# Performance work log

Hardware: AMD Instinct MI355X
Metric: run time of the kernel (lower is better)

Reference implementation:

```python
import jax, jax.numpy as jnp
import numpy as np

N_NODES = 100000
N_EDGES = 1600000
D_FEAT = 128


def setup_inputs() -> dict:
    key = jax.random.key(0)
    k1, k2, k3, k4 = jax.random.split(key, 4)
    support = jax.random.normal(k1, (N_NODES, D_FEAT), dtype=jnp.float32)
    vals = jax.random.uniform(k2, (N_EDGES,), dtype=jnp.float32)
    rows = jax.random.randint(k3, (N_EDGES,), 0, N_NODES, dtype=jnp.int64)
    cols = jax.random.randint(k4, (N_EDGES,), 0, N_NODES, dtype=jnp.int64)
    return {"support": support, "vals": vals, "rows": rows, "cols": cols}


def reference(support, vals, rows, cols):
    # out = adj @ support, adj given in COO: adj[rows[e], cols[e]] = vals[e]
    # Gather neighbor features, scale by edge weight, scatter-add to row nodes.
    msgs = vals[:, None] * support[cols]          # [E, F]
    out = jax.ops.segment_sum(msgs, rows, num_segments=support.shape[0])  # [N, F]
    return out
```

## Files before the change

kernel.cpp:

```cpp
#include <hip/hip_runtime.h>
#include <hip/hip_bf16.h>
#include <hip/hip_fp16.h>


#define D_FEAT 128
#define F4 32
#define H4 32
#define H8 16
#define STRIDE 64
#define OVF_CAP 131072
#define EPT 8
#define BINT 1024
#define NBINS 1024
#define CAP 2048
#define GMAXIT 4
#define BROWS 100
#define GT 512
#define CSRCAP (CAP + 64)

typedef float    vfloat4 __attribute__((ext_vector_type(4)));
typedef _Float16 half4v  __attribute__((ext_vector_type(4)));
typedef _Float16 half8v  __attribute__((ext_vector_type(8)));


__global__ __launch_bounds__(BINT) void
phase1_bin_kernel(const float4* __restrict__ support4,
                  half8v* __restrict__ supporth,
                  const int* __restrict__ rows,
                  const int* __restrict__ cols,
                  const float* __restrict__ vals,
                  int2* __restrict__ dense,
                  int* __restrict__ gcur,
                  int4* __restrict__ ovf,
                  int* __restrict__ ovf_count,
                  int E, int BT, int NBLK, int n8) {
    int b = blockIdx.x;
    int tid = threadIdx.x;

    if (b >= NBLK) {
        int m = (b - NBLK) * BINT + tid;
        if (m < n8) {
            float4 a0 = support4[(size_t)m * 2];
            float4 a1 = support4[(size_t)m * 2 + 1];
            half8v h;
            h[0] = (_Float16)a0.x; h[1] = (_Float16)a0.y;
            h[2] = (_Float16)a0.z; h[3] = (_Float16)a0.w;
            h[4] = (_Float16)a1.x; h[5] = (_Float16)a1.y;
            h[6] = (_Float16)a1.z; h[7] = (_Float16)a1.w;
            supporth[m] = h;
        }
        return;
    }

    __shared__ int  hist[NBINS];
    __shared__ int  off[NBINS + 1];
    __shared__ int  sstart[NBINS];
    __shared__ int2 sorted[BINT * EPT];

    for (int i = tid; i < NBINS; i += BINT) hist[i] = 0;
    __syncthreads();

    int t = b * BINT + tid;
    int   r[EPT];
    int   c[EPT];
    float v[EPT];
    int   rk[EPT];

    #pragma unroll
    for (int i = 0; i < EPT; ++i) {
        int e = t + i * BT;
        r[i] = (e < E) ? rows[e] : -1;
    }
    #pragma unroll
    for (int i = 0; i < EPT; ++i) {
        int e = t + i * BT;
        if (e < E) { c[i] = cols[e]; v[i] = vals[e]; }
    }
    #pragma unroll
    for (int i = 0; i < EPT; ++i)
        rk[i] = (r[i] >= 0) ? atomicAdd(&hist[r[i] / BROWS], 1) : 0;
    __syncthreads();

    if (tid < 64) {
        int l[16];
        int s = 0;
        #pragma unroll
        for (int k = 0; k < 16; ++k) {
            l[k] = hist[tid * 16 + k];
            s += l[k];
        }
        int inc = s;
        #pragma unroll
        for (int dd = 1; dd < 64; dd <<= 1) {
            int tt = __shfl_up(inc, dd, 64);
            if (tid >= dd) inc += tt;
        }
        int run = inc - s;
        #pragma unroll
        for (int k = 0; k < 16; ++k) {
            off[tid * 16 + k] = run;
            run += l[k];
        }
        if (tid == 63) off[NBINS] = run;
    }
    __syncthreads();

    #pragma unroll
    for (int i = 0; i < EPT; ++i) {
        if (r[i] < 0) continue;
        int d = r[i] / BROWS;
        int2 q;
        q.x = ((r[i] - d * BROWS) << 17) | c[i];
        q.y = __float_as_int(v[i]);
        sorted[off[d] + rk[i]] = q;
    }
    __syncthreads();

    {
        int l = off[tid + 1] - off[tid];
        sstart[tid] = (l > 0) ? atomicAdd(&gcur[tid], l) : 0;
    }
    __syncthreads();

    {
        int grp  = tid >> 4;
        int lane = tid & 15;
        for (int d = grp; d < NBINS; d += 64) {
            int o  = off[d];
            int l  = off[d + 1] - o;
            int st = sstart[d];
            for (int k = lane; k < l; k += 16) {
                int pos = st + k;
                int2 q = sorted[o + k];
                if (pos < CAP) {
                    dense[(size_t)d * CAP + pos] = q;
                } else {
                    int ox = atomicAdd(ovf_count, 1);
                    if (ox < OVF_CAP) {
                        int4 e4;
                        e4.x = d * BROWS + ((q.x >> 17) & 255);
                        e4.y = q.x & 0x1FFFF;
                        e4.z = q.y;
                        e4.w = 0;
                        ovf[ox] = e4;
                    }
                }
            }
        }
    }
}


__global__ __launch_bounds__(GT) void
bucket_csr_gather_kernel(const half8v* __restrict__ supporth,
                         const int2* __restrict__ dense,
                         const int* __restrict__ gcur,
                         const int4* __restrict__ ovf,
                         const int* __restrict__ ovf_count,
                         float4* __restrict__ out4, int N) {
    __shared__ __align__(16) int cnt[128];
    __shared__ __align__(16) int oc[128];
    __shared__ int oc2[128];
    __shared__ int off[129];
    __shared__ int2 csr[CSRCAP + 8];

    const int d   = blockIdx.x;
    const int tid = threadIdx.x;
    const int2* dbase = dense + (size_t)d * CAP;
    const int base = d * BROWS;

    int total = gcur[d];
    if (total > CAP) total = CAP;
    int ocnt = *ovf_count;
    if (ocnt > OVF_CAP) ocnt = OVF_CAP;

    if (tid < 128) { cnt[tid] = 0; oc[tid] = 0; oc2[tid] = 0; }
    __syncthreads();

    int2 ent[GMAXIT];
    int  err[GMAXIT];
    int  ernk[GMAXIT];
    #pragma unroll
    for (int it = 0; it < GMAXIT; ++it) {
        int s = tid + it * GT;
        err[it] = -1;
        if (s < total) {
            int2 q = dbase[s];
            int r = (q.x >> 17) & 255;
            ent[it].x = q.x & 0x1FFFF;
            ent[it].y = q.y;
            err[it] = r;
            ernk[it] = atomicAdd(&cnt[r], 1);
        }
    }
    if (ocnt > 0) {
        for (int i = tid; i < ocnt; i += GT) {
            int rr = ovf[i].x - base;
            if (rr >= 0 && rr < BROWS) atomicAdd(&oc[rr], 1);
        }
    }
    __syncthreads();

    if (tid < 32) {
        int4 c4 = ((int4*)cnt)[tid];
        int4 o4 = ((int4*)oc)[tid];
        int t0 = c4.x + o4.x;
        int t1 = t0 + c4.y + o4.y;
        int t2 = t1 + c4.z + o4.z;
        int t3 = t2 + c4.w + o4.w;
        int inc = t3;
        #pragma unroll
        for (int dd = 1; dd < 32; dd <<= 1) {
            int t = __shfl_up(inc, dd, 32);
            if (tid >= dd) inc += t;
        }
        int excl = inc - t3;
        off[tid * 4 + 0] = excl;
        off[tid * 4 + 1] = excl + t0;
        off[tid * 4 + 2] = excl + t1;
        off[tid * 4 + 3] = excl + t2;
        if (tid == 31) off[128] = inc;
    }
    __syncthreads();

    #pragma unroll
    for (int it = 0; it < GMAXIT; ++it) {
        if (err[it] >= 0)
            csr[off[err[it]] + ernk[it]] = ent[it];
    }
    if (ocnt > 0) {
        for (int i = tid; i < ocnt; i += GT) {
            int4 q = ovf[i];
            int rr = q.x - base;
            if (rr >= 0 && rr < BROWS) {
                int idx = off[rr] + cnt[rr] + atomicAdd(&oc2[rr], 1);
                if (idx < CSRCAP) { int2 e; e.x = q.y; e.y = q.z; csr[idx] = e; }
            }
        }
    }
    __syncthreads();

    const int g = tid >> 4;
    const int i = tid & 15;
    for (int rq = 0; rq < 4; ++rq) {
        int r = rq * 32 + g;
        if (r >= BROWS) continue;
        int beg = off[r];
        int end = off[r + 1];
        vfloat4 a00 = {0.f,0.f,0.f,0.f}, a01 = {0.f,0.f,0.f,0.f};
        vfloat4 a10 = {0.f,0.f,0.f,0.f}, a11 = {0.f,0.f,0.f,0.f};
        for (int k0 = beg; k0 < end; k0 += 8) {
            int   cc[8];
            float vv[8];
            #pragma unroll
            for (int u = 0; u < 8; ++u) {
                int2 e = csr[k0 + u];
                bool ib = (k0 + u) < end;
                cc[u] = ib ? e.x : 0;
                vv[u] = ib ? __int_as_float(e.y) : 0.f;
            }
            half8v s[8];
            #pragma unroll
            for (int u = 0; u < 8; ++u)
                s[u] = supporth[(size_t)cc[u] * H8 + i];
            #pragma unroll
            for (int u = 0; u < 8; ++u) {
                float v = vv[u];
                if (u & 1) {
                    a10.x += v * (float)s[u][0];
                    a10.y += v * (float)s[u][1];
                    a10.z += v * (float)s[u][2];
                    a10.w += v * (float)s[u][3];
                    a11.x += v * (float)s[u][4];
                    a11.y += v * (float)s[u][5];
                    a11.z += v * (float)s[u][6];
                    a11.w += v * (float)s[u][7];
                } else {
                    a00.x += v * (float)s[u][0];
                    a00.y += v * (float)s[u][1];
                    a00.z += v * (float)s[u][2];
                    a00.w += v * (float)s[u][3];
                    a01.x += v * (float)s[u][4];
                    a01.y += v * (float)s[u][5];
                    a01.z += v * (float)s[u][6];
                    a01.w += v * (float)s[u][7];
                }
            }
        }
        int row = base + r;
        if (row < N) {
            vfloat4 r0, r1;
            r0.x = a00.x + a10.x; r0.y = a00.y + a10.y;
            r0.z = a00.z + a10.z; r0.w = a00.w + a10.w;
            r1.x = a01.x + a11.x; r1.y = a01.y + a11.y;
            r1.z = a01.z + a11.z; r1.w = a01.w + a11.w;
            float4* dst = &out4[(size_t)row * F4 + (i << 1)];
            __builtin_nontemporal_store(r0, (vfloat4*)dst);
            __builtin_nontemporal_store(r1, (vfloat4*)(dst + 1));
        }
    }
}


__global__ void ovf_scatter_kernel(const float* __restrict__ support,
                                   const int4* __restrict__ ovf,
                                   const int* __restrict__ ovf_count,
                                   float* __restrict__ out, int cap) {
    int gid = blockIdx.x * blockDim.x + threadIdx.x;
    int i = gid >> 5;
    int j = gid & 31;
    int istride = (gridDim.x * blockDim.x) >> 5;
    int cnt = *ovf_count;
    if (cnt > cap) cnt = cap;
    for (; i < cnt; i += istride) {
        int4 q = ovf[i];
        float v = __int_as_float(q.z);
        const float4* s4 = (const float4*)support + (size_t)q.y * F4 + j;
        float4 s = *s4;
        float* o = out + (size_t)q.x * D_FEAT + j * 4;
        unsafeAtomicAdd(o + 0, v * s.x);
        unsafeAtomicAdd(o + 1, v * s.y);
        unsafeAtomicAdd(o + 2, v * s.z);
        unsafeAtomicAdd(o + 3, v * s.w);
    }
}


__global__ void convert_kernel(const float4* __restrict__ in,
                               half8v* __restrict__ out, int n8) {
    int t = blockIdx.x * blockDim.x + threadIdx.x;
    if (t >= n8) return;
    float4 a = in[(size_t)t * 2];
    float4 b = in[(size_t)t * 2 + 1];
    half8v h;
    h[0] = (_Float16)a.x; h[1] = (_Float16)a.y;
    h[2] = (_Float16)a.z; h[3] = (_Float16)a.w;
    h[4] = (_Float16)b.x; h[5] = (_Float16)b.y;
    h[6] = (_Float16)b.z; h[7] = (_Float16)b.w;
    out[t] = h;
}

__global__ void gather_half_kernel(const half4v* __restrict__ supporth,
                                   const int* __restrict__ cursor,
                                   const int2* __restrict__ pairs,
                                   float4* __restrict__ out4, int n_nodes) {
    unsigned int t = blockIdx.x * blockDim.x + threadIdx.x;
    unsigned int row = t >> 5;
    unsigned int j = t & 31;
    if (row >= (unsigned int)n_nodes) return;
    int deg = cursor[row];
    if (deg > STRIDE) deg = STRIDE;
    const int2* pr = pairs + (size_t)row * STRIDE;
    int2 z = {0, 0};
    int2 p0 = ((int)j < deg) ? pr[j] : z;
    int2 p1 = ((int)(j + 32) < deg) ? pr[j + 32] : z;
    int   c0 = p0.x;  float v0 = __int_as_float(p0.y);
    int   c1 = p1.x;  float v1 = __int_as_float(p1.y);
    int degr = (deg + 7) & ~7;
    float4 acc[4];
    #pragma unroll
    for (int u = 0; u < 4; ++u) acc[u] = {0.f, 0.f, 0.f, 0.f};
    for (int k = 0; k < degr; k += 8) {
        int   cc[8];
        float vv[8];
        #pragma unroll
        for (int u = 0; u < 8; ++u) {
            int kk = k + u;
            cc[u] = __shfl(kk < 32 ? c0 : c1, kk & 31, 32);
            vv[u] = __shfl(kk < 32 ? v0 : v1, kk & 31, 32);
        }
        half4v s[8];
        #pragma unroll
        for (int u = 0; u < 8; ++u)
            s[u] = supporth[(size_t)cc[u] * H4 + j];
        #pragma unroll
        for (int u = 0; u < 8; ++u) {
            acc[u & 3].x += vv[u] * (float)s[u][0];
            acc[u & 3].y += vv[u] * (float)s[u][1];
            acc[u & 3].z += vv[u] * (float)s[u][2];
            acc[u & 3].w += vv[u] * (float)s[u][3];
        }
    }
    vfloat4 res;
    res.x = (acc[0].x + acc[1].x) + (acc[2].x + acc[3].x);
    res.y = (acc[0].y + acc[1].y) + (acc[2].y + acc[3].y);
    res.z = (acc[0].z + acc[1].z) + (acc[2].z + acc[3].z);
    res.w = (acc[0].w + acc[1].w) + (acc[2].w + acc[3].w);
    __builtin_nontemporal_store(res, (vfloat4*)&out4[(size_t)row * F4 + j]);
}

__global__ void bucket_ilp_kernel(const int* __restrict__ rows,
                                  const int* __restrict__ cols,
                                  const float* __restrict__ vals,
                                  int* __restrict__ cursor,
                                  int* __restrict__ ovf_count,
                                  int2* __restrict__ pairs,
                                  int4* __restrict__ ovf,
                                  int n_edges, int gstride) {
    int tid = blockIdx.x * blockDim.x + threadIdx.x;
    int   r[EPT];
    int   c[EPT];
    float v[EPT];
    int   slot[EPT];
    #pragma unroll
    for (int i = 0; i < EPT; ++i) {
        int e = tid + i * gstride;
        r[i] = (e < n_edges) ? rows[e] : -1;
    }
    #pragma unroll
    for (int i = 0; i < EPT; ++i) {
        int e = tid + i * gstride;
        if (e < n_edges) { c[i] = cols[e]; v[i] = vals[e]; }
    }
    #pragma unroll
    for (int i = 0; i < EPT; ++i)
        slot[i] = (r[i] >= 0) ? atomicAdd(&cursor[r[i]], 1) : 0;
    #pragma unroll
    for (int i = 0; i < EPT; ++i) {
        if (r[i] < 0) continue;
        int2 p;
        p.x = c[i];
        p.y = __float_as_int(v[i]);
        if (slot[i] < STRIDE) {
            pairs[(size_t)r[i] * STRIDE + slot[i]] = p;
        } else {
            int o = atomicAdd(ovf_count, 1);
            if (o < OVF_CAP) {
                int4 q; q.x = r[i]; q.y = p.x; q.z = p.y; q.w = 0;
                ovf[o] = q;
            }
        }
    }
}


__global__ void gc_scatter_kernel(const float* __restrict__ support,
                                  const float* __restrict__ vals,
                                  const int* __restrict__ rows,
                                  const int* __restrict__ cols,
                                  float* __restrict__ out, int n_edges) {
    unsigned int t = blockIdx.x * blockDim.x + threadIdx.x;
    unsigned int e = t >> 5;
    unsigned int j = t & 31;
    if (e >= (unsigned int)n_edges) return;
    int r = rows[e];
    int c = cols[e];
    float v = vals[e];
    const float4* s4 = reinterpret_cast<const float4*>(support) + (size_t)c * F4 + j;
    float4 s = *s4;
    float* o = out + (size_t)r * D_FEAT + j * 4;
    unsafeAtomicAdd(o + 0, v * s.x);
    unsafeAtomicAdd(o + 1, v * s.y);
    unsafeAtomicAdd(o + 2, v * s.z);
    unsafeAtomicAdd(o + 3, v * s.w);
}


extern "C" void kernel_launch(void* const* d_in, const int* in_sizes, int n_in,
                              void* d_out, int out_size, void* d_ws, size_t ws_size,
                              hipStream_t stream) {
    const float* support = (const float*)d_in[0];
    const float* vals    = (const float*)d_in[1];
    const int*   rows    = (const int*)d_in[2];
    const int*   cols    = (const int*)d_in[3];
    float* out = (float*)d_out;

    int E = in_sizes[1];
    int N = in_sizes[0] / D_FEAT;
    int n8 = N * D_FEAT / 8;
    int ND = (N + BROWS - 1) / BROWS;
    int NBLK = (E + BINT * EPT - 1) / (BINT * EPT);
    int BT = NBLK * BINT;

    char* ws = (char*)d_ws;
    size_t cur = 0;
    auto carve = [&](size_t bytes) -> void* {
        void* p = ws + cur;
        cur += (bytes + 255) & ~(size_t)255;
        return p;
    };

    {
        size_t save = cur;
        int2*   dense     = (int2*)carve((size_t)NBINS * CAP * 8);
        int*    gcur      = (int*)carve((size_t)(NBINS + 256) * 4);
        int4*   ovf       = (int4*)carve((size_t)OVF_CAP * 16);
        half8v* supporth  = (half8v*)carve((size_t)N * D_FEAT * 2);
        if (cur <= ws_size && ND <= NBINS) {
            int* ovf_count = gcur + NBINS;
            (void)hipMemsetAsync(gcur, 0, (size_t)(NBINS + 1) * 4, stream);
            int cblocks = (n8 + BINT - 1) / BINT;
            phase1_bin_kernel<<<NBLK + cblocks, BINT, 0, stream>>>(
                (const float4*)support, supporth, rows, cols, vals,
                dense, gcur, ovf, ovf_count, E, BT, NBLK, n8);
            bucket_csr_gather_kernel<<<ND, GT, 0, stream>>>(
                supporth, dense, gcur, ovf, ovf_count, (float4*)out, N);
            return;
        }
        cur = save;
    }

    {
        size_t save = cur;
        int*    cursor   = (int*)carve((size_t)(N + 1) * 4);
        int2*   pairs    = (int2*)carve((size_t)N * STRIDE * 8);
        int4*   ovf      = (int4*)carve((size_t)8192 * 16);
        half8v* supporth = (half8v*)carve((size_t)N * D_FEAT * 2);
        if (cur <= ws_size) {
            int* ovf_count = cursor + N;
            int bthreads = (E + EPT - 1) / EPT;
            int bblocks = (bthreads + 255) / 256;
            int gstride = bblocks * 256;
            (void)hipMemsetAsync(cursor, 0, (size_t)(N + 1) * 4, stream);
            convert_kernel<<<(n8 + 255) / 256, 256, 0, stream>>>(
                (const float4*)support, supporth, n8);
            bucket_ilp_kernel<<<bblocks, 256, 0, stream>>>(
                rows, cols, vals, cursor, ovf_count, pairs, ovf, E, gstride);
            unsigned int gthreads = (unsigned int)N * 32;
            gather_half_kernel<<<(gthreads + 255) / 256, 256, 0, stream>>>(
                (const half4v*)supporth, cursor, pairs, (float4*)out, N);
            ovf_scatter_kernel<<<512, 256, 0, stream>>>(
                support, ovf, ovf_count, out, 8192);
            return;
        }
        cur = save;
    }

    (void)hipMemsetAsync(d_out, 0, (size_t)out_size * sizeof(float), stream);
    unsigned int total = (unsigned int)E * 32;
    gc_scatter_kernel<<<(total + 255) / 256, 256, 0, stream>>>(
        support, vals, rows, cols, out, E);
}
```

Measured before the change: 180.4 us.

## Scatter binned edges directly to global buckets, dropping shared-memory local sort

The binning phase no longer stages edges in a shared-memory sorted buffer with a prefix scan. Each thread now writes its edges straight to the global dense bucket, at the position given by the per-bin global atomic offset plus its local rank. The block size is halved to 512 threads. This removes the scan, two barriers and the large shared array, which should raise occupancy. The cost is that global writes are no longer grouped contiguously per bin, so they coalesce worse.

```diff
diff --git a/kernel.cpp b/kernel.cpp
--- a/kernel.cpp
+++ b/kernel.cpp
@@ -10,7 +10,7 @@
 #define STRIDE 64
 #define OVF_CAP 131072
 #define EPT 8
-#define BINT 1024
+#define BINT 512
 #define NBINS 1024
 #define CAP 2048
 #define GMAXIT 4
@@ -52,10 +52,8 @@
         return;
     }
 
-    __shared__ int  hist[NBINS];
-    __shared__ int  off[NBINS + 1];
-    __shared__ int  sstart[NBINS];
-    __shared__ int2 sorted[BINT * EPT];
+    __shared__ int hist[NBINS];
+    __shared__ int sstart[NBINS];
 
     for (int i = tid; i < NBINS; i += BINT) hist[i] = 0;
     __syncthreads();
@@ -81,27 +79,9 @@
         rk[i] = (r[i] >= 0) ? atomicAdd(&hist[r[i] / BROWS], 1) : 0;
     __syncthreads();
 
-    if (tid < 64) {
-        int l[16];
-        int s = 0;
-        #pragma unroll
-        for (int k = 0; k < 16; ++k) {
-            l[k] = hist[tid * 16 + k];
-            s += l[k];
-        }
-        int inc = s;
-        #pragma unroll
-        for (int dd = 1; dd < 64; dd <<= 1) {
-            int tt = __shfl_up(inc, dd, 64);
-            if (tid >= dd) inc += tt;
-        }
-        int run = inc - s;
-        #pragma unroll
-        for (int k = 0; k < 16; ++k) {
-            off[tid * 16 + k] = run;
-            run += l[k];
-        }
-        if (tid == 63) off[NBINS] = run;
+    for (int i = tid; i < NBINS; i += BINT) {
+        int l = hist[i];
+        sstart[i] = (l > 0) ? atomicAdd(&gcur[i], l) : 0;
     }
     __syncthreads();
 
@@ -109,42 +89,18 @@
     for (int i = 0; i < EPT; ++i) {
         if (r[i] < 0) continue;
         int d = r[i] / BROWS;
+        int pos = sstart[d] + rk[i];
         int2 q;
         q.x = ((r[i] - d * BROWS) << 17) | c[i];
         q.y = __float_as_int(v[i]);
-        sorted[off[d] + rk[i]] = q;
-    }
-    __syncthreads();
-
-    {
-        int l = off[tid + 1] - off[tid];
-        sstart[tid] = (l > 0) ? atomicAdd(&gcur[tid], l) : 0;
-    }
-    __syncthreads();
-
-    {
-        int grp  = tid >> 4;
-        int lane = tid & 15;
-        for (int d = grp; d < NBINS; d += 64) {
-            int o  = off[d];
-            int l  = off[d + 1] - o;
-            int st = sstart[d];
-            for (int k = lane; k < l; k += 16) {
-                int pos = st + k;
-                int2 q = sorted[o + k];
-                if (pos < CAP) {
-                    dense[(size_t)d * CAP + pos] = q;
-                } else {
-                    int ox = atomicAdd(ovf_count, 1);
-                    if (ox < OVF_CAP) {
-                        int4 e4;
-                        e4.x = d * BROWS + ((q.x >> 17) & 255);
-                        e4.y = q.x & 0x1FFFF;
-                        e4.z = q.y;
-                        e4.w = 0;
-                        ovf[ox] = e4;
-                    }
-                }
+        if (pos < CAP) {
+            dense[(size_t)d * CAP + pos] = q;
+        } else {
+            int ox = atomicAdd(ovf_count, 1);
+            if (ox < OVF_CAP) {
+                int4 e4;
+                e4.x = r[i]; e4.y = c[i]; e4.z = q.y; e4.w = 0;
+                ovf[ox] = e4;
             }
         }
     }
```

Measured after the change: 187.9 us. 1.04x slower.
